# Kernel tuning notes

Hardware: AMD Instinct MI355X
Metric: run time of the kernel (lower is better)

## Reference

```python
import jax, jax.numpy as jnp
import numpy as np

E, C, L, B = 8, 128, 1024, 32
FB = L // 2 + 1        # 513 freq bins
HD = 2 * FB            # 1026 hidden dim


def setup_inputs() -> dict:
    key = jax.random.key(0)
    ks = jax.random.split(key, 8)
    return {
        "X_time": jax.random.normal(ks[0], (B, C, L), jnp.float32),
        "bound_params": jax.random.normal(ks[1], (E - 1,), jnp.float32),
        "W1r": jax.random.normal(ks[2], (E, HD, FB), jnp.float32) * 0.1,
        "W1i": jax.random.normal(ks[3], (E, HD, FB), jnp.float32) * 0.1,
        "b1r": jnp.zeros((E, HD), jnp.float32),
        "b1i": jnp.zeros((E, HD), jnp.float32),
        "W2r": jax.random.normal(ks[4], (E, FB, HD), jnp.float32) * 0.1,
        "W2i": jax.random.normal(ks[5], (E, FB, HD), jnp.float32) * 0.1,
        "b2r": jnp.zeros((E, FB), jnp.float32),
        "b2i": jnp.zeros((E, FB), jnp.float32),
        "gate_W": jax.random.normal(ks[6], (E, FB), jnp.float32) * 0.1,
        "gate_b": jnp.zeros((E,), jnp.float32),
    }


def reference(X_time, bound_params, W1r, W1i, b1r, b1i, W2r, W2i, b2r, b2i, gate_W, gate_b):
    Bx, Cx, Lx = X_time.shape
    fb = Lx // 2 + 1
    e = W1r.shape[0]

    Xf = jnp.fft.rfft(X_time, axis=-1)                     # [B,C,FB] complex

    # learnable frequency-band binary masks
    raw = jax.nn.sigmoid(bound_params)
    bounds = jnp.sort(jnp.concatenate([jnp.zeros(1, raw.dtype), raw, jnp.ones(1, raw.dtype)]))
    idx = (bounds * (fb - 1)).astype(jnp.int32)
    starts = idx[:e]
    ends = jnp.concatenate([idx[1:e], jnp.array([fb], jnp.int32)])
    pos = jnp.arange(fb)
    masks = ((pos[None, :] >= starts[:, None]) & (pos[None, :] < ends[:, None])).astype(X_time.dtype)  # [E,FB]

    # masked spectra per expert, split into real/imag: [E,B,C,FB]
    m = masks[:, None, None, :]
    xr = Xf.real * m
    xi = Xf.imag * m

    # expert layer 1: complex linear (W [E,HD,FB]) + complex ReLU
    hr = jnp.einsum('ehf,ebcf->ebch', W1r, xr) - jnp.einsum('ehf,ebcf->ebch', W1i, xi) + b1r[:, None, None, :]
    hi = jnp.einsum('ehf,ebcf->ebch', W1r, xi) + jnp.einsum('ehf,ebcf->ebch', W1i, xr) + b1i[:, None, None, :]
    hr = jax.nn.relu(hr)
    hi = jax.nn.relu(hi)

    # expert layer 2: complex linear (W [E,FB,HD]) -> [E,B,C,FB]
    yr = jnp.einsum('efh,ebch->ebcf', W2r, hr) - jnp.einsum('efh,ebch->ebcf', W2i, hi) + b2r[:, None, None, :]
    yi = jnp.einsum('efh,ebch->ebcf', W2r, hi) + jnp.einsum('efh,ebch->ebcf', W2i, hr) + b2i[:, None, None, :]

    # gate: mean |Xf| over channels -> linear -> softmax over experts
    mag = jnp.mean(jnp.abs(Xf), axis=1)                    # [B,FB]
    gate = jax.nn.softmax(mag @ gate_W.T + gate_b, axis=-1)  # [B,E]

    comb_r = jnp.einsum('ebcf,be->bcf', yr, gate)
    comb_i = jnp.einsum('ebcf,be->bcf', yi, gate)
    return jnp.fft.irfft(jax.lax.complex(comb_r, comb_i), n=Lx, axis=-1)
```

## Files before the change

kernel.cpp:

```cpp
#include <hip/hip_runtime.h>
#include <hip/hip_bf16.h>
#include <math.h>

typedef __hip_bfloat16 bf16;
typedef __attribute__((ext_vector_type(8))) short short8;
typedef __attribute__((ext_vector_type(4))) short short4v;
typedef __attribute__((ext_vector_type(4))) float f32x4;

#define FB 513
#define HD 1026
#define NN 1024
#define MR 4096
#define NE 8
#define BATCH 32

#define XINT_LD 1056
#define HP_LD   2080
#define B1_ROWS 2176
#define B2_ROWS 1152
#define KCAT    16640
#define PLANE   ((size_t)MR * XINT_LD)

__device__ __forceinline__ void gload16(const void* g, void* l) {
    __builtin_amdgcn_global_load_lds((const __attribute__((address_space(1))) void*)g,
                                     (__attribute__((address_space(3))) void*)l, 16, 0, 0);
}
__device__ __forceinline__ bf16 f2b(float v) { return __float2bfloat16(v); }
__device__ __forceinline__ unsigned short f2bu(float v) {
    bf16 b = __float2bfloat16(v);
    return *reinterpret_cast<unsigned short*>(&b);
}
__device__ __forceinline__ float bu2f(unsigned short u) {
    return __uint_as_float(((unsigned)u) << 16);
}
__device__ __forceinline__ unsigned pack2(float a, float b) {
    return (unsigned)f2bu(a) | ((unsigned)f2bu(b) << 16);
}

__device__ __forceinline__ void xcd_swizzle(int* px, int* py) {
    int gx = gridDim.x;
    int orig = blockIdx.x + gx * blockIdx.y;
    int q = (gx * gridDim.y) >> 3;
    int wg = (orig & 7) * q + (orig >> 3);
    *px = wg % gx;
    *py = wg / gx;
}

__global__ void prep_kernel(const float* __restrict__ bp, int* __restrict__ se) {
    if (threadIdx.x == 0 && blockIdx.x == 0) {
        float b[9];
        b[0] = 0.0f; b[8] = 1.0f;
        for (int i = 0; i < 7; i++) b[i + 1] = 1.0f / (1.0f + expf(-bp[i]));
        for (int i = 1; i < 9; i++) { float v = b[i]; int j = i - 1;
            while (j >= 0 && b[j] > v) { b[j + 1] = b[j]; j--; } b[j + 1] = v; }
        int idx[9];
        for (int i = 0; i < 9; i++) idx[i] = (int)(b[i] * (float)(FB - 1));
        for (int e = 0; e < NE; e++) {
            se[2 * e] = idx[e];
            se[2 * e + 1] = (e < NE - 1) ? idx[e + 1] : FB;
        }
    }
}

#define N_FF  (1056L * 1024)
#define N_FI  (1024L * 1056)
#define N_B1P ((long)NE * B1_ROWS * (XINT_LD/2))
#define N_B2P ((long)(B2_ROWS/2) * KCAT)
#define N_XP  ((long)MR * NN / 2)
#define N_PREP (N_FF + N_FI + N_B1P + N_B2P + N_XP)

__global__ void prep_bulk(const float* __restrict__ W1r, const float* __restrict__ W1i,
                          const float* __restrict__ W2r, const float* __restrict__ W2i,
                          const float* __restrict__ X, const int* __restrict__ se,
                          bf16* __restrict__ Ffwd, bf16* __restrict__ Finv,
                          bf16* __restrict__ B1, bf16* __restrict__ B2,
                          bf16* __restrict__ Xb) {
    long i = (long)blockIdx.x * 256 + threadIdx.x;
    const float TWO_PI = 6.283185307179586f;
    if (i < N_FF) {
        int n = (int)(i >> 10), t = (int)(i & (NN - 1));
        float v = 0.0f;
        if (n < 2 * FB) {
            int f = n >> 1, k = (f * t) & (NN - 1);
            float s, c; sincosf(TWO_PI * (float)k / (float)NN, &s, &c);
            v = (n & 1) ? -s : c;
        }
        Ffwd[i] = f2b(v);
        return;
    }
    i -= N_FF;
    if (i < N_FI) {
        int t = (int)(i / XINT_LD), k = (int)(i % XINT_LD);
        float v = 0.0f;
        if (k < 2 * FB) {
            int f = k >> 1, kk = (f * t) & (NN - 1);
            float s, c; sincosf(TWO_PI * (float)kk / (float)NN, &s, &c);
            float cf = (f == 0 || f == FB - 1) ? 1.0f : 2.0f;
            float sc = cf * (1.0f / (float)NN);
            v = (k & 1) ? -s * sc : c * sc;
        }
        Finv[i] = f2b(v);
        return;
    }
    i -= N_FI;
    if (i < N_B1P) {
        int f = (int)(i % (XINT_LD / 2));
        long t = i / (XINT_LD / 2);
        int n = (int)(t % B1_ROWS);
        int e = (int)(t / B1_ROWS);
        float ve = 0.0f, vo = 0.0f;
        if (n < 2 * HD && f < FB && f >= se[2 * e] && f < se[2 * e + 1]) {
            int hi_part = (n >= HD);
            int h = hi_part ? n - HD : n;
            long wi = ((long)e * HD + h) * FB + f;
            float wr = W1r[wi], wim = W1i[wi];
            ve = hi_part ? wim : wr;
            vo = hi_part ? wr : -wim;
        }
        *(unsigned*)(B1 + ((size_t)(e * B1_ROWS + n)) * XINT_LD + 2 * f) = pack2(ve, vo);
        return;
    }
    i -= N_B1P;
    if (i < N_B2P) {
        int col = (int)(i % KCAT);
        int f = (int)(i / KCAT);
        int e = col / HP_LD, k = col % HP_LD;
        float vr = 0.0f, vi_ = 0.0f;
        if (f < FB && k < 2 * HD) {
            int hi_part = (k >= HD);
            int h = hi_part ? k - HD : k;
            long wi = ((long)e * FB + f) * HD + h;
            float wr = W2r[wi], wim = W2i[wi];
            vr  = hi_part ? -wim : wr;
            vi_ = hi_part ? wr : wim;
        }
        B2[(size_t)(2 * f) * KCAT + col]     = f2b(vr);
        B2[(size_t)(2 * f + 1) * KCAT + col] = f2b(vi_);
        return;
    }
    i -= N_B2P;
    if (i < N_XP) {
        float2 v = ((const float2*)X)[i];
        *(unsigned*)(Xb + 2 * i) = pack2(v.x, v.y);
    }
}

#define MAG_LD 520
__global__ void mag_kernel(const bf16* __restrict__ Xint, float* __restrict__ magp) {
    int b = blockIdx.x, g = blockIdx.y, t = threadIdx.x;
    float acc[3] = {0.0f, 0.0f, 0.0f};
    const bf16* base = Xint + ((size_t)b * 128 + g * 16) * XINT_LD;
    for (int c = 0; c < 16; c++) {
        const bf16* row = base + (size_t)c * XINT_LD;
#pragma unroll
        for (int kk = 0; kk < 3; kk++) {
            int f = t + 256 * kk;
            if (f < FB) {
                float xr = __bfloat162float(row[2 * f]);
                float xi = __bfloat162float(row[2 * f + 1]);
                acc[kk] += sqrtf(xr * xr + xi * xi);
            }
        }
    }
#pragma unroll
    for (int kk = 0; kk < 3; kk++) {
        int f = t + 256 * kk;
        if (f < FB) magp[((size_t)b * 8 + g) * MAG_LD + f] = acc[kk];
    }
}

__global__ void gate_bias_kernel(const float* __restrict__ magp, const float* __restrict__ gW,
                                 const float* __restrict__ gb, const float* __restrict__ b2r,
                                 const float* __restrict__ b2i, float* __restrict__ gate,
                                 float* __restrict__ biasC) {
    __shared__ float sred[256];
    __shared__ float sg[8];
    int b = blockIdx.x, tid = threadIdx.x;
    int e = tid & 7, j = tid >> 3;
    float acc = 0.0f;
    for (int f = j; f < FB; f += 32) {
        float m = 0.0f;
#pragma unroll
        for (int g = 0; g < 8; g++) m += magp[((size_t)b * 8 + g) * MAG_LD + f];
        acc += m * (1.0f / 128.0f) * gW[e * FB + f];
    }
    sred[tid] = acc;
    __syncthreads();
    if (tid < 64) {
        float a = sred[tid] + sred[tid + 64] + sred[tid + 128] + sred[tid + 192];
        a += __shfl_xor(a, 8); a += __shfl_xor(a, 16); a += __shfl_xor(a, 32);
        float logit = a + gb[e];
        float mx = logit;
        mx = fmaxf(mx, __shfl_xor(mx, 1)); mx = fmaxf(mx, __shfl_xor(mx, 2)); mx = fmaxf(mx, __shfl_xor(mx, 4));
        float ex = expf(logit - mx);
        float sum = ex;
        sum += __shfl_xor(sum, 1); sum += __shfl_xor(sum, 2); sum += __shfl_xor(sum, 4);
        if (tid < 8) { float g_ = ex / sum; sg[tid] = g_; gate[b * NE + tid] = g_; }
    }
    __syncthreads();
    for (int c = tid; c < XINT_LD; c += 256) {
        float v = 0.0f;
        if (c < 2 * FB) {
            int f = c >> 1;
            const float* bb = (c & 1) ? b2i : b2r;
#pragma unroll
            for (int ee = 0; ee < NE; ee++) v += sg[ee] * bb[ee * FB + f];
        }
        biasC[b * XINT_LD + c] = v;
    }
}

__global__ void reduce_f32(const float* __restrict__ planes, bf16* __restrict__ outp) {
    long idx = (long)blockIdx.x * 256 + threadIdx.x;
    if (idx >= (long)MR * (XINT_LD / 4)) return;
    int c4 = (int)(idx % (XINT_LD / 4));
    long r = idx / (XINT_LD / 4);
    int c0 = c4 * 4;
    size_t base = (size_t)r * XINT_LD + c0;
    float4 a = *(const float4*)(planes + base);
    float4 b = *(const float4*)(planes + PLANE + base);
    float s[4] = {a.x + b.x, a.y + b.y, a.z + b.z, a.w + b.w};
    short4v o;
#pragma unroll
    for (int j = 0; j < 4; j++) o[j] = (short)f2bu((c0 + j < 2 * FB) ? s[j] : 0.0f);
    *(short4v*)(outp + base) = o;
}

__global__ void reduce_bf(const bf16* __restrict__ planes, const float* __restrict__ biasC,
                          bf16* __restrict__ outp) {
    long idx = (long)blockIdx.x * 256 + threadIdx.x;
    if (idx >= (long)MR * (XINT_LD / 8)) return;
    int c8 = (int)(idx % (XINT_LD / 8));
    long r = idx / (XINT_LD / 8);
    int c0 = c8 * 8;
    size_t base = (size_t)r * XINT_LD + c0;
    float s[8] = {};
#pragma unroll
    for (int z = 0; z < 4; z++) {
        short8 v = *(const short8*)(planes + (size_t)z * PLANE + base);
#pragma unroll
        for (int j = 0; j < 8; j++) s[j] += bu2f((unsigned short)v[j]);
    }
    const float* bC = biasC + ((int)(r >> 7)) * XINT_LD + c0;
    short8 o;
#pragma unroll
    for (int j = 0; j < 8; j++) {
        float val = (c0 + j < 2 * FB) ? (s[j] + bC[j]) : 0.0f;
        o[j] = (short)f2bu(val);
    }
    *(short8*)(outp + base) = o;
}

__global__ void reduce_out(const float* __restrict__ planes, float* __restrict__ out) {
    long idx = (long)blockIdx.x * 256 + threadIdx.x;
    if (idx >= (long)MR * NN / 4) return;
    size_t base = (size_t)idx * 4;
    float4 a = *(const float4*)(planes + base);
    float4 b = *(const float4*)(planes + (size_t)MR * NN + base);
    float4 o = {a.x + b.x, a.y + b.y, a.z + b.z, a.w + b.w};
    *(float4*)(out + base) = o;
}

template <int EPI>
__global__ void gemm_mfma(const bf16* __restrict__ A, int lda,
                          const bf16* __restrict__ B, int ldb, size_t zBstride,
                          void* __restrict__ Cv, int ldc, size_t zCoff,
                          int N, int K, int kPerZ,
                          const int* __restrict__ se2,
                          const float* __restrict__ biasR, const float* __restrict__ biasI,
                          int zBias, const float* __restrict__ gate8) {
    __shared__ bf16 As[128 * 32];
    __shared__ bf16 Bs[128 * 32];
    int tid = threadIdx.x;
    int zz = blockIdx.z;
    int bx, by;
    xcd_swizzle(&bx, &by);
    int row0 = by * 128, col0 = bx * 128;
    const bf16* Bz = B + (size_t)zz * zBstride;

    int kS, kE;
    if (EPI == 1) { int s = se2[2 * zz], e = se2[2 * zz + 1]; kS = (2 * s) & ~31; kE = (2 * e + 31) & ~31; }
    else          { kS = zz * kPerZ; kE = min(K, kS + kPerZ); }

    f32x4 acc[4][4] = {};

    int lane = tid & 63, wid = tid >> 6;
    int wrB = (wid >> 1) << 6, wcB = (wid & 1) << 6;
    int lr = lane & 15, lk = (lane >> 4) << 3;

    int r_a = tid >> 2, c_a = (tid & 3) << 3;
    int r_b = (tid + 256) >> 2, c_b = ((tid + 256) & 3) << 3;

    for (int kt = kS; kt < kE; kt += 32) {
        gload16(A + (size_t)(row0 + r_a) * lda + kt + c_a, &As[(size_t)tid * 8]);
        gload16(A + (size_t)(row0 + r_b) * lda + kt + c_b, &As[((size_t)tid + 256) * 8]);
        gload16(Bz + (size_t)(col0 + r_a) * ldb + kt + c_a, &Bs[(size_t)tid * 8]);
        gload16(Bz + (size_t)(col0 + r_b) * ldb + kt + c_b, &Bs[((size_t)tid + 256) * 8]);
        __syncthreads();
        short8 av[4], bv[4];
#pragma unroll
        for (int m = 0; m < 4; m++)
            av[m] = *(const short8*)&As[(wrB + m * 16 + lr) * 32 + lk];
#pragma unroll
        for (int n = 0; n < 4; n++)
            bv[n] = *(const short8*)&Bs[(wcB + n * 16 + lr) * 32 + lk];
#pragma unroll
        for (int m = 0; m < 4; m++)
#pragma unroll
            for (int n = 0; n < 4; n++)
                acc[m][n] = __builtin_amdgcn_mfma_f32_16x16x32_bf16(av[m], bv[n], acc[m][n], 0, 0, 0);
        __syncthreads();
    }

    int r0 = row0 + wrB + ((lane >> 4) << 2);
    int c0i = col0 + wcB + (lane & 15);
    float g = (EPI == 1) ? gate8[(row0 >> 7) * NE + zz] : 0.0f;

#pragma unroll
    for (int m = 0; m < 4; m++)
#pragma unroll
        for (int n = 0; n < 4; n++) {
            int c = c0i + n * 16;
            if (c >= N) continue;
#pragma unroll
            for (int j = 0; j < 4; j++) {
                int r = r0 + m * 16 + j;
                float v = acc[m][n][j];
                if (EPI == 0) {
                    ((bf16*)Cv + (size_t)zz * zCoff)[(size_t)r * ldc + c] = f2b(v);
                } else if (EPI == 1) {
                    v += (c < HD) ? biasR[zz * zBias + c] : biasI[zz * zBias + c - HD];
                    v = fmaxf(v, 0.0f) * g;
                    ((bf16*)Cv + (size_t)zz * zCoff)[(size_t)r * ldc + c] = f2b(v);
                } else {
                    ((float*)Cv + (size_t)zz * zCoff)[(size_t)r * ldc + c] = v;
                }
            }
        }
}

extern "C" void kernel_launch(void* const* d_in, const int* in_sizes, int n_in,
                              void* d_out, int out_size, void* d_ws, size_t ws_size,
                              hipStream_t stream) {
    const float* X   = (const float*)d_in[0];
    const float* bp  = (const float*)d_in[1];
    const float* W1r = (const float*)d_in[2];
    const float* W1i = (const float*)d_in[3];
    const float* b1r = (const float*)d_in[4];
    const float* b1i = (const float*)d_in[5];
    const float* W2r = (const float*)d_in[6];
    const float* W2i = (const float*)d_in[7];
    const float* b2r = (const float*)d_in[8];
    const float* b2i = (const float*)d_in[9];
    const float* gW  = (const float*)d_in[10];
    const float* gb  = (const float*)d_in[11];
    float* out = (float*)d_out;

    const size_t SZH = (size_t)MR * HP_LD * 2;
    const size_t PARTIAL_BYTES = 2 * PLANE * 4;

    char* wsb = (char*)d_ws;
    char* p = wsb;
    auto alloc = [&](size_t bytes) -> char* {
        char* r = p; p += (bytes + 255) & ~255ULL; return r;
    };
    int*   se    = (int*)alloc(64 * 4);
    float* magp  = (float*)alloc((size_t)BATCH * 8 * MAG_LD * 4);
    float* gate  = (float*)alloc((size_t)BATCH * NE * 4);
    float* biasC = (float*)alloc((size_t)BATCH * XINT_LD * 4);
    bf16*  Ffwd  = (bf16*)alloc(1056 * 1024 * 2);
    bf16*  Finv  = (bf16*)alloc((size_t)NN * XINT_LD * 2);
    bf16*  B1    = (bf16*)alloc((size_t)NE * B1_ROWS * XINT_LD * 2);
    bf16*  B2    = (bf16*)alloc((size_t)B2_ROWS * KCAT * 2);
    bf16*  Xint  = (bf16*)alloc(PLANE * 2);
    bf16*  combb = (bf16*)alloc(PLANE * 2);
    char*  partialSlot = alloc(PARTIAL_BYTES);
    float* partialF = (float*)partialSlot;
    bf16*  partialB = (bf16*)partialSlot;

    size_t used = (size_t)(p - wsb);
    int chunk = (used + 8 * SZH <= ws_size) ? 8 : 4;
    bf16* Hp = (bf16*)alloc((size_t)chunk * SZH);
    bf16* Xb = (bf16*)((char*)Hp + (size_t)chunk * SZH - (size_t)MR * NN * 2);

    prep_kernel<<<1, 64, 0, stream>>>(bp, se);
    prep_bulk<<<(unsigned)((N_PREP + 255) / 256), 256, 0, stream>>>(
        W1r, W1i, W2r, W2i, X, se, Ffwd, Finv, B1, B2, Xb);

    gemm_mfma<3><<<dim3(9, 32, 2), 256, 0, stream>>>(
        Xb, NN, Ffwd, NN, 0, partialF, XINT_LD, PLANE,
        1056, NN, 512, nullptr, nullptr, nullptr, 0, nullptr);
    reduce_f32<<<(unsigned)(((size_t)MR * (XINT_LD / 4) + 255) / 256), 256, 0, stream>>>(
        partialF, Xint);

    mag_kernel<<<dim3(BATCH, 8), 256, 0, stream>>>(Xint, magp);
    gate_bias_kernel<<<BATCH, 256, 0, stream>>>(magp, gW, gb, b2r, b2i, gate, biasC);

    int nch = NE / chunk;
    for (int ci = 0; ci < nch; ci++) {
        int e0 = ci * chunk;
        gemm_mfma<1><<<dim3(17, 32, chunk), 256, 0, stream>>>(
            Xint, XINT_LD,
            B1 + (size_t)e0 * B1_ROWS * XINT_LD, XINT_LD, (size_t)B1_ROWS * XINT_LD,
            Hp, chunk * HP_LD, HP_LD,
            2 * HD, 0, 0,
            se + 2 * e0, b1r + (size_t)e0 * HD, b1i + (size_t)e0 * HD, HD, gate + e0);

        int Kc = chunk * HP_LD;
        int zsplit = (chunk == 8) ? 4 : 2;
        int kPerZ = Kc / zsplit;
        gemm_mfma<0><<<dim3(9, 32, zsplit), 256, 0, stream>>>(
            Hp, Kc, B2 + (size_t)e0 * HP_LD, KCAT, 0,
            partialB + (size_t)(ci * zsplit) * PLANE, XINT_LD, PLANE,
            2 * FB, Kc, kPerZ, nullptr, nullptr, nullptr, 0, nullptr);
    }

    reduce_bf<<<(unsigned)(((size_t)MR * (XINT_LD / 8) + 255) / 256), 256, 0, stream>>>(
        partialB, biasC, combb);

    gemm_mfma<3><<<dim3(8, 32, 2), 256, 0, stream>>>(
        combb, XINT_LD, Finv, XINT_LD, 0, partialF, NN, (size_t)MR * NN,
        NN, XINT_LD, 544, nullptr, nullptr, nullptr, 0, nullptr);
    reduce_out<<<(unsigned)(((size_t)MR * NN / 4 + 255) / 256), 256, 0, stream>>>(
        partialF, out);
}
```

Measured before the change: 448.5 us.

## Fold inverse DFT into layer-2 weights and use 256x256 MFMA GEMM

Precomputes a combined matrix from the layer-2 expert weights and the inverse DFT basis, so the second expert GEMM writes time-domain output directly. This removes the separate combine-reduce and inverse-FFT GEMM stages. The output bias is likewise moved to time domain by a small kernel. A new 512-thread, 256x256-tile double-buffered MFMA GEMM with LDS swizzling handles both the weight-fold product and the main split-K product. The cost is an extra weight-preparation GEMM on every call, plus bf16 rounding of the folded weights, which may change accuracy.

```diff
diff --git a/kernel.cpp b/kernel.cpp
--- a/kernel.cpp
+++ b/kernel.cpp
@@ -15,11 +15,12 @@
 #define BATCH 32
 
 #define XINT_LD 1056
+#define FINV_LD 1088
 #define HP_LD   2080
 #define B1_ROWS 2176
-#define B2_ROWS 1152
 #define KCAT    16640
 #define PLANE   ((size_t)MR * XINT_LD)
+#define MAG_LD  520
 
 __device__ __forceinline__ void gload16(const void* g, void* l) {
     __builtin_amdgcn_global_load_lds((const __attribute__((address_space(1))) void*)g,
@@ -63,17 +64,17 @@
 }
 
 #define N_FF  (1056L * 1024)
-#define N_FI  (1024L * 1056)
-#define N_B1P ((long)NE * B1_ROWS * (XINT_LD/2))
-#define N_B2P ((long)(B2_ROWS/2) * KCAT)
+#define N_FI  (1024L * FINV_LD)
+#define N_B1P ((long)NE * B1_ROWS * (XINT_LD / 2))
+#define N_B2T ((long)KCAT * (FINV_LD / 2))
 #define N_XP  ((long)MR * NN / 2)
-#define N_PREP (N_FF + N_FI + N_B1P + N_B2P + N_XP)
+#define N_PREP (N_FF + N_FI + N_B1P + N_B2T + N_XP)
 
 __global__ void prep_bulk(const float* __restrict__ W1r, const float* __restrict__ W1i,
                           const float* __restrict__ W2r, const float* __restrict__ W2i,
                           const float* __restrict__ X, const int* __restrict__ se,
                           bf16* __restrict__ Ffwd, bf16* __restrict__ Finv,
-                          bf16* __restrict__ B1, bf16* __restrict__ B2,
+                          bf16* __restrict__ B1, bf16* __restrict__ B2t,
                           bf16* __restrict__ Xb) {
     long i = (long)blockIdx.x * 256 + threadIdx.x;
     const float TWO_PI = 6.283185307179586f;
@@ -90,7 +91,7 @@
     }
     i -= N_FF;
     if (i < N_FI) {
-        int t = (int)(i / XINT_LD), k = (int)(i % XINT_LD);
+        int t = (int)(i / FINV_LD), k = (int)(i % FINV_LD);
         float v = 0.0f;
         if (k < 2 * FB) {
             int f = k >> 1, kk = (f * t) & (NN - 1);
@@ -121,31 +122,29 @@
         return;
     }
     i -= N_B1P;
-    if (i < N_B2P) {
-        int col = (int)(i % KCAT);
-        int f = (int)(i / KCAT);
-        int e = col / HP_LD, k = col % HP_LD;
+    if (i < N_B2T) {
+        int fp = (int)(i % (FINV_LD / 2));
+        int k = (int)(i / (FINV_LD / 2));
+        int e = k / HP_LD, kk2 = k % HP_LD;
         float vr = 0.0f, vi_ = 0.0f;
-        if (f < FB && k < 2 * HD) {
-            int hi_part = (k >= HD);
-            int h = hi_part ? k - HD : k;
-            long wi = ((long)e * FB + f) * HD + h;
+        if (fp < FB && kk2 < 2 * HD) {
+            int hi_part = (kk2 >= HD);
+            int h = hi_part ? kk2 - HD : kk2;
+            long wi = ((long)e * FB + fp) * HD + h;
             float wr = W2r[wi], wim = W2i[wi];
             vr  = hi_part ? -wim : wr;
             vi_ = hi_part ? wr : wim;
         }
-        B2[(size_t)(2 * f) * KCAT + col]     = f2b(vr);
-        B2[(size_t)(2 * f + 1) * KCAT + col] = f2b(vi_);
+        *(unsigned*)(B2t + (size_t)k * FINV_LD + 2 * fp) = pack2(vr, vi_);
         return;
     }
-    i -= N_B2P;
+    i -= N_B2T;
     if (i < N_XP) {
         float2 v = ((const float2*)X)[i];
         *(unsigned*)(Xb + 2 * i) = pack2(v.x, v.y);
     }
 }
 
-#define MAG_LD 520
 __global__ void mag_kernel(const bf16* __restrict__ Xint, float* __restrict__ magp) {
     int b = blockIdx.x, g = blockIdx.y, t = threadIdx.x;
     float acc[3] = {0.0f, 0.0f, 0.0f};
@@ -172,7 +171,7 @@
 __global__ void gate_bias_kernel(const float* __restrict__ magp, const float* __restrict__ gW,
                                  const float* __restrict__ gb, const float* __restrict__ b2r,
                                  const float* __restrict__ b2i, float* __restrict__ gate,
-                                 float* __restrict__ biasC) {
+                                 float* __restrict__ biasCs) {
     __shared__ float sred[256];
     __shared__ float sg[8];
     int b = blockIdx.x, tid = threadIdx.x;
@@ -205,9 +204,21 @@
             const float* bb = (c & 1) ? b2i : b2r;
 #pragma unroll
             for (int ee = 0; ee < NE; ee++) v += sg[ee] * bb[ee * FB + f];
-        }
-        biasC[b * XINT_LD + c] = v;
-    }
+            float cf = (f == 0 || f == FB - 1) ? 1.0f : 2.0f;
+            v *= cf * (1.0f / (float)NN);
+        }
+        biasCs[b * XINT_LD + c] = v;
+    }
+}
+
+__global__ void biasT_kernel(const float* __restrict__ biasCs, const bf16* __restrict__ Ffwd,
+                             float* __restrict__ biasT) {
+    int t = blockIdx.x * 256 + threadIdx.x;
+    int b = blockIdx.y;
+    float s = 0.0f;
+    for (int c = 0; c < 2 * FB; c++)
+        s += biasCs[b * XINT_LD + c] * __bfloat162float(Ffwd[(size_t)c * NN + t]);
+    biasT[b * NN + t] = s;
 }
 
 __global__ void reduce_f32(const float* __restrict__ planes, bf16* __restrict__ outp) {
@@ -226,39 +237,25 @@
     *(short4v*)(outp + base) = o;
 }
 
-__global__ void reduce_bf(const bf16* __restrict__ planes, const float* __restrict__ biasC,
-                          bf16* __restrict__ outp) {
+__global__ void reduce_out4(const bf16* __restrict__ planes, const float* __restrict__ biasT,
+                            float* __restrict__ out) {
     long idx = (long)blockIdx.x * 256 + threadIdx.x;
-    if (idx >= (long)MR * (XINT_LD / 8)) return;
-    int c8 = (int)(idx % (XINT_LD / 8));
-    long r = idx / (XINT_LD / 8);
-    int c0 = c8 * 8;
-    size_t base = (size_t)r * XINT_LD + c0;
+    if (idx >= (long)MR * NN / 8) return;
+    size_t base = (size_t)idx * 8;
+    long r = base >> 10;
+    int t = (int)(base & (NN - 1));
     float s[8] = {};
 #pragma unroll
     for (int z = 0; z < 4; z++) {
-        short8 v = *(const short8*)(planes + (size_t)z * PLANE + base);
+        short8 v = *(const short8*)(planes + (size_t)z * MR * NN + base);
 #pragma unroll
         for (int j = 0; j < 8; j++) s[j] += bu2f((unsigned short)v[j]);
     }
-    const float* bC = biasC + ((int)(r >> 7)) * XINT_LD + c0;
-    short8 o;
-#pragma unroll
-    for (int j = 0; j < 8; j++) {
-        float val = (c0 + j < 2 * FB) ? (s[j] + bC[j]) : 0.0f;
-        o[j] = (short)f2bu(val);
-    }
-    *(short8*)(outp + base) = o;
-}
-
-__global__ void reduce_out(const float* __restrict__ planes, float* __restrict__ out) {
-    long idx = (long)blockIdx.x * 256 + threadIdx.x;
-    if (idx >= (long)MR * NN / 4) return;
-    size_t base = (size_t)idx * 4;
-    float4 a = *(const float4*)(planes + base);
-    float4 b = *(const float4*)(planes + (size_t)MR * NN + base);
-    float4 o = {a.x + b.x, a.y + b.y, a.z + b.z, a.w + b.w};
-    *(float4*)(out + base) = o;
+    const float* bT = biasT + (r >> 7) * NN + t;
+    float4 o0 = {s[0] + bT[0], s[1] + bT[1], s[2] + bT[2], s[3] + bT[3]};
+    float4 o1 = {s[4] + bT[4], s[5] + bT[5], s[6] + bT[6], s[7] + bT[7]};
+    *(float4*)(out + base) = o0;
+    *(float4*)(out + base + 4) = o1;
 }
 
 template <int EPI>
@@ -326,9 +323,7 @@
             for (int j = 0; j < 4; j++) {
                 int r = r0 + m * 16 + j;
                 float v = acc[m][n][j];
-                if (EPI == 0) {
-                    ((bf16*)Cv + (size_t)zz * zCoff)[(size_t)r * ldc + c] = f2b(v);
-                } else if (EPI == 1) {
+                if (EPI == 1) {
                     v += (c < HD) ? biasR[zz * zBias + c] : biasI[zz * zBias + c - HD];
                     v = fmaxf(v, 0.0f) * g;
                     ((bf16*)Cv + (size_t)zz * zCoff)[(size_t)r * ldc + c] = f2b(v);
@@ -337,6 +332,132 @@
                 }
             }
         }
+}
+
+__device__ __forceinline__ void stage_half(const bf16* gbase, int ld, int kt,
+                                           bf16* ldsBase, int tid) {
+#pragma unroll
+    for (int j = 0; j < 2; j++) {
+        int r = j * 64 + (tid >> 3);
+        int sc = ((tid & 7) ^ ((tid >> 3) & 7)) * 8;
+        gload16(gbase + (size_t)r * ld + kt + sc, ldsBase + j * 4096 + tid * 8);
+    }
+}
+
+#define MF(a, b, c) __builtin_amdgcn_mfma_f32_16x16x32_bf16(a, b, c, 0, 0, 0)
+#define RD(off) (*(const short8*)(bc + (off)))
+
+#define PHASE_MFMA(FM)                                                        \
+    {                                                                         \
+        short8 aa0 = RD(aBase + (FM) * 1024 + cb0);                           \
+        short8 aa1 = RD(aBase + (FM) * 1024 + cb1);                           \
+        short8 ab0 = RD(aBase + (FM + 1) * 1024 + cb0);                       \
+        short8 ab1 = RD(aBase + (FM + 1) * 1024 + cb1);                       \
+        __builtin_amdgcn_s_setprio(1);                                        \
+        acc[FM][0] = MF(aa0, b0[0], acc[FM][0]);                              \
+        acc[FM][0] = MF(aa1, b1[0], acc[FM][0]);                              \
+        acc[FM][1] = MF(aa0, b0[1], acc[FM][1]);                              \
+        acc[FM][1] = MF(aa1, b1[1], acc[FM][1]);                              \
+        acc[FM][2] = MF(aa0, b0[2], acc[FM][2]);                              \
+        acc[FM][2] = MF(aa1, b1[2], acc[FM][2]);                              \
+        acc[FM][3] = MF(aa0, b0[3], acc[FM][3]);                              \
+        acc[FM][3] = MF(aa1, b1[3], acc[FM][3]);                              \
+        acc[FM + 1][0] = MF(ab0, b0[0], acc[FM + 1][0]);                      \
+        acc[FM + 1][0] = MF(ab1, b1[0], acc[FM + 1][0]);                      \
+        acc[FM + 1][1] = MF(ab0, b0[1], acc[FM + 1][1]);                      \
+        acc[FM + 1][1] = MF(ab1, b1[1], acc[FM + 1][1]);                      \
+        acc[FM + 1][2] = MF(ab0, b0[2], acc[FM + 1][2]);                      \
+        acc[FM + 1][2] = MF(ab1, b1[2], acc[FM + 1][2]);                      \
+        acc[FM + 1][3] = MF(ab0, b0[3], acc[FM + 1][3]);                      \
+        acc[FM + 1][3] = MF(ab1, b1[3], acc[FM + 1][3]);                      \
+        __builtin_amdgcn_s_setprio(0);                                        \
+        __builtin_amdgcn_sched_barrier(0);                                    \
+        __builtin_amdgcn_s_barrier();                                         \
+    }
+
+template <int SWZ>
+__global__ __launch_bounds__(512, 2) void gemm8p(
+        const bf16* __restrict__ A, int lda, const bf16* __restrict__ B, int ldb,
+        bf16* __restrict__ C, int ldc, size_t zCoff,
+        int tilesPerZ, int totTiles, int gx) {
+    __shared__ bf16 sm[65536];
+    int tid = threadIdx.x;
+    int id = blockIdx.x;
+    int bx, by, z;
+    if (SWZ == 1) {
+        int by_z = (id & 7) * 8 + (id >> 5);
+        bx = (id >> 3) & 3;
+        z = by_z >> 4;
+        by = by_z & 15;
+    } else {
+        bx = id % gx; by = id / gx; z = 0;
+    }
+    int row0 = by * 256, col0 = bx * 256;
+    int t0 = z * tilesPerZ;
+    int nt = min(tilesPerZ, totTiles - t0);
+    int kS = t0 * 64;
+
+    const bf16* Ab = A + (size_t)row0 * lda;
+    const bf16* Bb = B + (size_t)col0 * ldb;
+
+    stage_half(Ab, lda, kS, sm, tid);
+    stage_half(Ab + (size_t)128 * lda, lda, kS, sm + 8192, tid);
+    stage_half(Bb, ldb, kS, sm + 16384, tid);
+    stage_half(Bb + (size_t)128 * ldb, ldb, kS, sm + 24576, tid);
+
+    f32x4 acc[8][4] = {};
+
+    int l = tid & 63, w = tid >> 6;
+    int wm = w >> 2, wn = w & 3;
+    int lr = l & 15, lk4 = l >> 4;
+    int swz = lr & 7;
+    int cb0 = ((lk4) ^ swz) * 8;
+    int cb1 = ((4 + lk4) ^ swz) * 8;
+    int aBaseR = wm * 8192 + lr * 64;
+    int bBaseR = 16384 + (wn >> 1) * 8192 + (wn & 1) * 4096 + lr * 64;
+
+    for (int t = 0; t < nt; ++t) {
+        const int cur = t & 1;
+        const bf16* bc = sm + cur * 32768;
+        bf16* bufN = sm + (cur ^ 1) * 32768;
+        int aBase = aBaseR, bBase = bBaseR;
+        int ktn = kS + (t + 1) * 64;
+        bool more = (t + 1) < nt;
+        if (more) {
+            stage_half(Ab, lda, ktn, bufN, tid);
+            stage_half(Ab + (size_t)128 * lda, lda, ktn, bufN + 8192, tid);
+            asm volatile("s_waitcnt vmcnt(4)" ::: "memory");
+        } else {
+            asm volatile("s_waitcnt vmcnt(0)" ::: "memory");
+        }
+        __builtin_amdgcn_s_barrier();
+        __builtin_amdgcn_sched_barrier(0);
+        short8 b0[4], b1[4];
+#pragma unroll
+        for (int n = 0; n < 4; n++) {
+            b0[n] = RD(bBase + n * 1024 + cb0);
+            b1[n] = RD(bBase + n * 1024 + cb1);
+        }
+        PHASE_MFMA(0)
+        if (more) {
+            stage_half(Bb, ldb, ktn, bufN + 16384, tid);
+            stage_half(Bb + (size_t)128 * ldb, ldb, ktn, bufN + 24576, tid);
+        }
+        PHASE_MFMA(2)
+        PHASE_MFMA(4)
+        PHASE_MFMA(6)
+    }
+
+    bf16* Cp = C + (size_t)z * zCoff;
+    int rb = row0 + wm * 128 + lk4 * 4;
+    int cbase = col0 + wn * 64 + lr;
+#pragma unroll
+    for (int fm = 0; fm < 8; fm++)
+#pragma unroll
+        for (int n = 0; n < 4; n++)
+#pragma unroll
+            for (int j = 0; j < 4; j++)
+                Cp[(size_t)(rb + fm * 16 + j) * ldc + cbase + n * 16] = f2b(acc[fm][n][j]);
 }
 
 extern "C" void kernel_launch(void* const* d_in, const int* in_sizes, int n_in,
@@ -357,70 +478,53 @@
     float* out = (float*)d_out;
 
     const size_t SZH = (size_t)MR * HP_LD * 2;
-    const size_t PARTIAL_BYTES = 2 * PLANE * 4;
-
-    char* wsb = (char*)d_ws;
-    char* p = wsb;
+
+    char* p = (char*)d_ws;
     auto alloc = [&](size_t bytes) -> char* {
         char* r = p; p += (bytes + 255) & ~255ULL; return r;
     };
-    int*   se    = (int*)alloc(64 * 4);
-    float* magp  = (float*)alloc((size_t)BATCH * 8 * MAG_LD * 4);
-    float* gate  = (float*)alloc((size_t)BATCH * NE * 4);
-    float* biasC = (float*)alloc((size_t)BATCH * XINT_LD * 4);
-    bf16*  Ffwd  = (bf16*)alloc(1056 * 1024 * 2);
-    bf16*  Finv  = (bf16*)alloc((size_t)NN * XINT_LD * 2);
-    bf16*  B1    = (bf16*)alloc((size_t)NE * B1_ROWS * XINT_LD * 2);
-    bf16*  B2    = (bf16*)alloc((size_t)B2_ROWS * KCAT * 2);
-    bf16*  Xint  = (bf16*)alloc(PLANE * 2);
-    bf16*  combb = (bf16*)alloc(PLANE * 2);
-    char*  partialSlot = alloc(PARTIAL_BYTES);
-    float* partialF = (float*)partialSlot;
-    bf16*  partialB = (bf16*)partialSlot;
-
-    size_t used = (size_t)(p - wsb);
-    int chunk = (used + 8 * SZH <= ws_size) ? 8 : 4;
-    bf16* Hp = (bf16*)alloc((size_t)chunk * SZH);
-    bf16* Xb = (bf16*)((char*)Hp + (size_t)chunk * SZH - (size_t)MR * NN * 2);
+    int*   se     = (int*)alloc(64 * 4);
+    float* magp   = (float*)alloc((size_t)BATCH * 8 * MAG_LD * 4);
+    float* gate   = (float*)alloc((size_t)BATCH * NE * 4);
+    float* biasCs = (float*)alloc((size_t)BATCH * XINT_LD * 4);
+    float* biasT  = (float*)alloc((size_t)BATCH * NN * 4);
+    bf16*  Ffwd   = (bf16*)alloc(1056 * 1024 * 2);
+    bf16*  Finv   = (bf16*)alloc((size_t)NN * FINV_LD * 2);
+    bf16*  B1     = (bf16*)alloc((size_t)NE * B1_ROWS * XINT_LD * 2);
+    bf16*  B2t    = (bf16*)alloc((size_t)KCAT * FINV_LD * 2);
+    bf16*  Xint   = (bf16*)alloc(PLANE * 2);
+    char*  planes = alloc(2 * PLANE * 4);
+    bf16*  Hp     = (bf16*)alloc(8 * SZH);
+    float* planesF = (float*)planes;
+    bf16*  planesB = (bf16*)planes;
+    bf16*  B2inv  = (bf16*)B1;
+    bf16*  Xb     = (bf16*)((char*)Hp + 8 * SZH - (size_t)MR * NN * 2);
 
     prep_kernel<<<1, 64, 0, stream>>>(bp, se);
     prep_bulk<<<(unsigned)((N_PREP + 255) / 256), 256, 0, stream>>>(
-        W1r, W1i, W2r, W2i, X, se, Ffwd, Finv, B1, B2, Xb);
+        W1r, W1i, W2r, W2i, X, se, Ffwd, Finv, B1, B2t, Xb);
 
     gemm_mfma<3><<<dim3(9, 32, 2), 256, 0, stream>>>(
-        Xb, NN, Ffwd, NN, 0, partialF, XINT_LD, PLANE,
+        Xb, NN, Ffwd, NN, 0, planesF, XINT_LD, PLANE,
         1056, NN, 512, nullptr, nullptr, nullptr, 0, nullptr);
     reduce_f32<<<(unsigned)(((size_t)MR * (XINT_LD / 4) + 255) / 256), 256, 0, stream>>>(
-        partialF, Xint);
+        planesF, Xint);
 
     mag_kernel<<<dim3(BATCH, 8), 256, 0, stream>>>(Xint, magp);
-    gate_bias_kernel<<<BATCH, 256, 0, stream>>>(magp, gW, gb, b2r, b2i, gate, biasC);
-
-    int nch = NE / chunk;
-    for (int ci = 0; ci < nch; ci++) {
-        int e0 = ci * chunk;
-        gemm_mfma<1><<<dim3(17, 32, chunk), 256, 0, stream>>>(
-            Xint, XINT_LD,
-            B1 + (size_t)e0 * B1_ROWS * XINT_LD, XINT_LD, (size_t)B1_ROWS * XINT_LD,
-            Hp, chunk * HP_LD, HP_LD,
-            2 * HD, 0, 0,
-            se + 2 * e0, b1r + (size_t)e0 * HD, b1i + (size_t)e0 * HD, HD, gate + e0);
-
-        int Kc = chunk * HP_LD;
-        int zsplit = (chunk == 8) ? 4 : 2;
-        int kPerZ = Kc / zsplit;
-        gemm_mfma<0><<<dim3(9, 32, zsplit), 256, 0, stream>>>(
-            Hp, Kc, B2 + (size_t)e0 * HP_LD, KCAT, 0,
-            partialB + (size_t)(ci * zsplit) * PLANE, XINT_LD, PLANE,
-            2 * FB, Kc, kPerZ, nullptr, nullptr, nullptr, 0, nullptr);
-    }
-
-    reduce_bf<<<(unsigned)(((size_t)MR * (XINT_LD / 8) + 255) / 256), 256, 0, stream>>>(
-        partialB, biasC, combb);
-
-    gemm_mfma<3><<<dim3(8, 32, 2), 256, 0, stream>>>(
-        combb, XINT_LD, Finv, XINT_LD, 0, partialF, NN, (size_t)MR * NN,
-        NN, XINT_LD, 544, nullptr, nullptr, nullptr, 0, nullptr);
-    reduce_out<<<(unsigned)(((size_t)MR * NN / 4 + 255) / 256), 256, 0, stream>>>(
-        partialF, out);
-}
+    gate_bias_kernel<<<BATCH, 256, 0, stream>>>(magp, gW, gb, b2r, b2i, gate, biasCs);
+    biasT_kernel<<<dim3(4, BATCH), 256, 0, stream>>>(biasCs, Ffwd, biasT);
+
+    gemm_mfma<1><<<dim3(17, 32, 8), 256, 0, stream>>>(
+        Xint, XINT_LD, B1, XINT_LD, (size_t)B1_ROWS * XINT_LD,
+        Hp, NE * HP_LD, HP_LD, 2 * HD, 0, 0,
+        se, b1r, b1i, HD, gate);
+
+    gemm8p<0><<<260, 512, 0, stream>>>(
+        Finv, FINV_LD, B2t, FINV_LD, B2inv, KCAT, 0, 17, 17, 65);
+
+    gemm8p<1><<<256, 512, 0, stream>>>(
+        Hp, KCAT, B2inv, KCAT, planesB, NN, (size_t)MR * NN, 65, 260, 4);
+
+    reduce_out4<<<(unsigned)(((size_t)MR * NN / 8 + 255) / 256), 256, 0, stream>>>(
+        planesB, biasT, out);
+}
```

New measurement: 470.6 us. 4.9% more time.
